# Kernel tuning notes

Measured on AMD Instinct MI355X. Metric: run time of the kernel, lower is better.

## Reference

```python
import jax, jax.numpy as jnp
import numpy as np
import math

B, C = 512, 100000
H_PARAM = 0.333
S_PARAM = 64.0
M_PARAM = 0.4
T_ALPHA = 1.0
EPS = 1e-06


def setup_inputs() -> dict:
    key = jax.random.key(0)
    k1, k2, k3 = jax.random.split(key, 3)
    # cosine similarities in (-1, 1)
    logits = jax.random.uniform(k1, (B, C), dtype=jnp.float32, minval=-1.0, maxval=1.0)
    # embedding L2 norms: positive, roughly in a realistic range ~[5, 45]
    norms = jax.random.uniform(k2, (B, 1), dtype=jnp.float32, minval=5.0, maxval=45.0)
    labels = jax.random.randint(k3, (B,), 0, C, dtype=jnp.int64)
    return {"logits": logits, "norms": norms, "labels": labels}


def reference(logits, norms, labels):
    # t_alpha = 1.0 in training mode => batch_mean/std buffers equal the
    # current batch statistics exactly (torch.std is unbiased, ddof=1).
    cosine = jnp.clip(logits, -1.0 + EPS, 1.0 - EPS)              # [B, C]
    safe_norms = jax.lax.stop_gradient(jnp.clip(norms, 0.001, 100.0))  # [B, 1]

    mean = jnp.mean(safe_norms)
    std = jnp.std(safe_norms, ddof=1)

    margin_scaler = (safe_norms - mean) / (std + EPS) * H_PARAM   # [B, 1]
    margin_scaler = jnp.clip(margin_scaler, -1.0, 1.0)

    onehot = jax.nn.one_hot(labels, C, dtype=cosine.dtype)        # [B, C]

    g_angular = -M_PARAM * margin_scaler                          # [B, 1]
    theta = jnp.arccos(cosine)                                    # [B, C]
    theta_m = jnp.clip(theta + onehot * g_angular, EPS, math.pi - EPS)

    g_add = M_PARAM + M_PARAM * margin_scaler                     # [B, 1]
    cosine_m_final = jnp.cos(theta_m) - onehot * g_add            # [B, C]
    scaled = cosine_m_final * S_PARAM

    # mean cross-entropy over the batch
    logp = jax.nn.log_softmax(scaled, axis=-1)                    # [B, C]
    nll = -jnp.take_along_axis(logp, labels[:, None], axis=1)[:, 0]
    return jnp.mean(nll)
```

## Files before the change

### kernel.cpp

```cpp
#include <hip/hip_runtime.h>
#include <math.h>

#define B_SZ 512
#define C_SZ 100000
#define H_PARAM 0.333f
#define S_PARAM 64.0f
#define M_PARAM 0.4f
#define EPS 1e-6f
#define PI_F 3.14159265358979323846f

#define CHUNKS_PER_ROW 4
#define F4_PER_ROW (C_SZ / 4)
#define F4_PER_CHUNK (F4_PER_ROW / CHUNKS_PER_ROW)

__device__ inline float waveReduceSum(float v) {
#pragma unroll
    for (int off = 32; off > 0; off >>= 1) v += __shfl_xor(v, off, 64);
    return v;
}

__device__ inline float clip1(float x) {
    return fminf(fmaxf(x, -1.0f + EPS), 1.0f - EPS);
}

__global__ __launch_bounds__(512) void stats_kernel(
    const float* __restrict__ norms,
    const float* __restrict__ logits,
    const int* __restrict__ labels,
    float* __restrict__ target,
    float* __restrict__ plain,
    float* __restrict__ acc) {
    __shared__ float sh[8];
    int i = threadIdx.x;
    float n = fminf(fmaxf(norms[i], 0.001f), 100.0f);

    int wave = i >> 6, lane = i & 63;
    float wsum = waveReduceSum(n);
    if (lane == 0) sh[wave] = wsum;
    __syncthreads();
    float total = 0.f;
#pragma unroll
    for (int w = 0; w < 8; ++w) total += sh[w];
    float mean = total * (1.0f / 512.0f);
    __syncthreads();

    float d = n - mean;
    float wss = waveReduceSum(d * d);
    if (lane == 0) sh[wave] = wss;
    __syncthreads();
    float tss = 0.f;
#pragma unroll
    for (int w = 0; w < 8; ++w) tss += sh[w];
    float sd = sqrtf(tss / 511.0f);

    float ms = (n - mean) / (sd + EPS) * H_PARAM;
    ms = fminf(fmaxf(ms, -1.0f), 1.0f);
    float g_ang = -M_PARAM * ms;
    float g_add = M_PARAM + M_PARAM * ms;

    int lab = labels[i];
    float c = clip1(logits[(size_t)i * C_SZ + lab]);
    float theta = acosf(c);
    float tm = fminf(fmaxf(theta + g_ang, EPS), PI_F - EPS);
    float t = (cosf(tm) - g_add) * S_PARAM;

    target[i] = t;
    plain[i] = __expf(S_PARAM * c - S_PARAM);
    acc[i] = 0.f;
}

__global__ __launch_bounds__(256) void row_kernel(
    const float* __restrict__ logits,
    float* __restrict__ acc) {
    int row = blockIdx.x >> 2;
    int chunk = blockIdx.x & 3;
    const float4* lr4 = (const float4*)(logits + (size_t)row * C_SZ);
    int begin = chunk * F4_PER_CHUNK;
    int end = begin + F4_PER_CHUNK;

    float l = 0.f;
    for (int j = begin + threadIdx.x; j < end; j += 256) {
        float4 v = lr4[j];
        l += __expf(fmaf(S_PARAM, clip1(v.x), -S_PARAM));
        l += __expf(fmaf(S_PARAM, clip1(v.y), -S_PARAM));
        l += __expf(fmaf(S_PARAM, clip1(v.z), -S_PARAM));
        l += __expf(fmaf(S_PARAM, clip1(v.w), -S_PARAM));
    }

    __shared__ float shl[4];
    int wave = threadIdx.x >> 6, lane = threadIdx.x & 63;
    float wsum = waveReduceSum(l);
    if (lane == 0) shl[wave] = wsum;
    __syncthreads();
    if (threadIdx.x == 0) {
        atomicAdd(&acc[row], shl[0] + shl[1] + shl[2] + shl[3]);
    }
}

__global__ __launch_bounds__(512) void final_kernel(
    const float* __restrict__ acc,
    const float* __restrict__ target,
    const float* __restrict__ plain,
    float* __restrict__ out) {
    __shared__ float sh[8];
    int i = threadIdx.x;
    float t = target[i];
    float s = acc[i] - plain[i] + __expf(t - S_PARAM);
    float v = S_PARAM + logf(s) - t;

    int wave = i >> 6, lane = i & 63;
    float wsum = waveReduceSum(v);
    if (lane == 0) sh[wave] = wsum;
    __syncthreads();
    if (i == 0) {
        float total = 0.f;
#pragma unroll
        for (int w = 0; w < 8; ++w) total += sh[w];
        out[0] = total * (1.0f / 512.0f);
    }
}

extern "C" void kernel_launch(void* const* d_in, const int* in_sizes, int n_in,
                              void* d_out, int out_size, void* d_ws, size_t ws_size,
                              hipStream_t stream) {
    const float* logits = (const float*)d_in[0];
    const float* norms  = (const float*)d_in[1];
    const int*   labels = (const int*)d_in[2];
    float* out = (float*)d_out;

    float* target = (float*)d_ws;
    float* plain  = target + B_SZ;
    float* acc    = plain + B_SZ;

    stats_kernel<<<1, 512, 0, stream>>>(norms, logits, labels, target, plain, acc);
    row_kernel<<<B_SZ * CHUNKS_PER_ROW, 256, 0, stream>>>(logits, acc);
    final_kernel<<<1, 512, 0, stream>>>(acc, target, plain, out);
}
```

Before: 289.5 us.

## Fold stats kernel into final kernel and replace atomics with per-chunk partials

Removes the separate single-block stats kernel by computing norm statistics and the target logit inside the final kernel, cutting one launch from the serial chain. Row partial sums are now written to a per-block array instead of being accumulated with atomicAdd, which also removes the need to zero the accumulator first. Rows are split into 8 chunks instead of 4 to launch more blocks for the streaming pass. The final kernel does a bit more serial work on one block.

```diff
diff --git a/kernel.cpp b/kernel.cpp
--- a/kernel.cpp
+++ b/kernel.cpp
@@ -9,7 +9,7 @@
 #define EPS 1e-6f
 #define PI_F 3.14159265358979323846f
 
-#define CHUNKS_PER_ROW 4
+#define CHUNKS_PER_ROW 8
 #define F4_PER_ROW (C_SZ / 4)
 #define F4_PER_CHUNK (F4_PER_ROW / CHUNKS_PER_ROW)
 
@@ -23,57 +23,11 @@
     return fminf(fmaxf(x, -1.0f + EPS), 1.0f - EPS);
 }
 
-__global__ __launch_bounds__(512) void stats_kernel(
-    const float* __restrict__ norms,
-    const float* __restrict__ logits,
-    const int* __restrict__ labels,
-    float* __restrict__ target,
-    float* __restrict__ plain,
-    float* __restrict__ acc) {
-    __shared__ float sh[8];
-    int i = threadIdx.x;
-    float n = fminf(fmaxf(norms[i], 0.001f), 100.0f);
-
-    int wave = i >> 6, lane = i & 63;
-    float wsum = waveReduceSum(n);
-    if (lane == 0) sh[wave] = wsum;
-    __syncthreads();
-    float total = 0.f;
-#pragma unroll
-    for (int w = 0; w < 8; ++w) total += sh[w];
-    float mean = total * (1.0f / 512.0f);
-    __syncthreads();
-
-    float d = n - mean;
-    float wss = waveReduceSum(d * d);
-    if (lane == 0) sh[wave] = wss;
-    __syncthreads();
-    float tss = 0.f;
-#pragma unroll
-    for (int w = 0; w < 8; ++w) tss += sh[w];
-    float sd = sqrtf(tss / 511.0f);
-
-    float ms = (n - mean) / (sd + EPS) * H_PARAM;
-    ms = fminf(fmaxf(ms, -1.0f), 1.0f);
-    float g_ang = -M_PARAM * ms;
-    float g_add = M_PARAM + M_PARAM * ms;
-
-    int lab = labels[i];
-    float c = clip1(logits[(size_t)i * C_SZ + lab]);
-    float theta = acosf(c);
-    float tm = fminf(fmaxf(theta + g_ang, EPS), PI_F - EPS);
-    float t = (cosf(tm) - g_add) * S_PARAM;
-
-    target[i] = t;
-    plain[i] = __expf(S_PARAM * c - S_PARAM);
-    acc[i] = 0.f;
-}
-
 __global__ __launch_bounds__(256) void row_kernel(
     const float* __restrict__ logits,
-    float* __restrict__ acc) {
-    int row = blockIdx.x >> 2;
-    int chunk = blockIdx.x & 3;
+    float* __restrict__ partial) {
+    int row = blockIdx.x >> 3;
+    int chunk = blockIdx.x & 7;
     const float4* lr4 = (const float4*)(logits + (size_t)row * C_SZ);
     int begin = chunk * F4_PER_CHUNK;
     int end = begin + F4_PER_CHUNK;
@@ -93,30 +47,66 @@
     if (lane == 0) shl[wave] = wsum;
     __syncthreads();
     if (threadIdx.x == 0) {
-        atomicAdd(&acc[row], shl[0] + shl[1] + shl[2] + shl[3]);
+        partial[blockIdx.x] = shl[0] + shl[1] + shl[2] + shl[3];
     }
 }
 
 __global__ __launch_bounds__(512) void final_kernel(
-    const float* __restrict__ acc,
-    const float* __restrict__ target,
-    const float* __restrict__ plain,
+    const float* __restrict__ norms,
+    const float* __restrict__ logits,
+    const int* __restrict__ labels,
+    const float* __restrict__ partial,
     float* __restrict__ out) {
     __shared__ float sh[8];
     int i = threadIdx.x;
-    float t = target[i];
-    float s = acc[i] - plain[i] + __expf(t - S_PARAM);
+    int wave = i >> 6, lane = i & 63;
+
+    float n = fminf(fmaxf(norms[i], 0.001f), 100.0f);
+    float wsum = waveReduceSum(n);
+    if (lane == 0) sh[wave] = wsum;
+    __syncthreads();
+    float total = 0.f;
+#pragma unroll
+    for (int w = 0; w < 8; ++w) total += sh[w];
+    float mean = total * (1.0f / 512.0f);
+    __syncthreads();
+
+    float d = n - mean;
+    float wss = waveReduceSum(d * d);
+    if (lane == 0) sh[wave] = wss;
+    __syncthreads();
+    float tss = 0.f;
+#pragma unroll
+    for (int w = 0; w < 8; ++w) tss += sh[w];
+    float sd = sqrtf(tss / 511.0f);
+    __syncthreads();
+
+    float ms = (n - mean) / (sd + EPS) * H_PARAM;
+    ms = fminf(fmaxf(ms, -1.0f), 1.0f);
+    float g_ang = -M_PARAM * ms;
+    float g_add = M_PARAM + M_PARAM * ms;
+
+    int lab = labels[i];
+    float c = clip1(logits[(size_t)i * C_SZ + lab]);
+    float theta = acosf(c);
+    float tm = fminf(fmaxf(theta + g_ang, EPS), PI_F - EPS);
+    float t = (cosf(tm) - g_add) * S_PARAM;
+    float plain = __expf(S_PARAM * c - S_PARAM);
+
+    float s = 0.f;
+#pragma unroll
+    for (int k = 0; k < CHUNKS_PER_ROW; ++k) s += partial[i * CHUNKS_PER_ROW + k];
+    s = s - plain + __expf(t - S_PARAM);
     float v = S_PARAM + logf(s) - t;
 
-    int wave = i >> 6, lane = i & 63;
-    float wsum = waveReduceSum(v);
-    if (lane == 0) sh[wave] = wsum;
+    float vsum = waveReduceSum(v);
+    if (lane == 0) sh[wave] = vsum;
     __syncthreads();
     if (i == 0) {
-        float total = 0.f;
+        float tot = 0.f;
 #pragma unroll
-        for (int w = 0; w < 8; ++w) total += sh[w];
-        out[0] = total * (1.0f / 512.0f);
+        for (int w = 0; w < 8; ++w) tot += sh[w];
+        out[0] = tot * (1.0f / 512.0f);
     }
 }
 
@@ -128,11 +118,8 @@
     const int*   labels = (const int*)d_in[2];
     float* out = (float*)d_out;
 
-    float* target = (float*)d_ws;
-    float* plain  = target + B_SZ;
-    float* acc    = plain + B_SZ;
+    float* partial = (float*)d_ws;
 
-    stats_kernel<<<1, 512, 0, stream>>>(norms, logits, labels, target, plain, acc);
-    row_kernel<<<B_SZ * CHUNKS_PER_ROW, 256, 0, stream>>>(logits, acc);
-    final_kernel<<<1, 512, 0, stream>>>(acc, target, plain, out);
+    row_kernel<<<B_SZ * CHUNKS_PER_ROW, 256, 0, stream>>>(logits, partial);
+    final_kernel<<<1, 512, 0, stream>>>(norms, logits, labels, partial, out);
 }
```

After: 282.6 us. 2.4% less time.
